# Kernel optimization log

Hardware: AMD Instinct MI355X
Metric: run time of the kernel (lower is better)

## Reference

```python
import jax, jax.numpy as jnp
import numpy as np

EPS = 1e-8
H = 4      # n_heads
W = 64     # mem_word_length


def _split_controls(controls):
    # per-head partition: [W, W, W, 1, 1, 3, 1]
    B = controls.shape[0]
    sizes = [W, W, W, 1, 1, 3, 1]
    parts, pos = [], 0
    for s in sizes:
        n = H * s
        parts.append(controls[:, pos:pos + n].reshape(B, H, s))
        pos += n
    return parts  # keys, erase_vec, write_vec, betas, gates, shifts, gammas


def _address_memory(memory, keys, betas, gates, shifts, gammas, prev_weights):
    keys = jnp.tanh(keys)                      # [B,H,W]
    betas = jax.nn.softplus(betas)             # [B,H,1]
    gates = jax.nn.sigmoid(gates)              # [B,H,1]
    shifts = jax.nn.softmax(shifts, axis=-1)   # [B,H,3]
    gammas = 1.0 + jax.nn.softplus(gammas)     # [B,H,1]

    # cosine similarity: [B,H,N]
    dots = jnp.einsum('bhw,bnw->bhn', keys, memory)
    norm = jnp.linalg.norm(keys, axis=-1, keepdims=True) \
         * jnp.linalg.norm(memory, axis=-1)[:, None, :]
    scores = dots / (norm + EPS)

    w_content = jax.nn.softmax(scores * betas, axis=-1)            # [B,H,N]
    w_interp = gates * w_content + (1.0 - gates) * prev_weights    # [B,H,N]

    # circular 3-tap shift: out[n] = s0*w[n-1] + s1*w[n] + s2*w[n+1]
    w_shift = (shifts[..., 0:1] * jnp.roll(w_interp, 1, axis=-1)
             + shifts[..., 1:2] * w_interp
             + shifts[..., 2:3] * jnp.roll(w_interp, -1, axis=-1))

    w_sharp = w_shift ** gammas
    return w_sharp / (jnp.sum(w_sharp, axis=-1, keepdims=True) + EPS)


def reference(memory, controls, prev_weights):
    keys, erase_vec, write_vec, betas, gates, shifts, gammas = _split_controls(controls)
    write_dist = _address_memory(memory, keys, betas, gates, shifts, gammas, prev_weights)  # [B,H,N]
    write_data = jnp.tanh(write_vec)       # [B,H,W]
    erase_data = jax.nn.sigmoid(erase_vec) # [B,H,W]

    # erase: prod over heads of (1 - w[b,h,n]*e[b,h,w]) -> [B,N,W]
    erase_matrix = jnp.prod(1.0 - write_dist[:, :, :, None] * erase_data[:, :, None, :], axis=1)
    update_matrix = jnp.einsum('bhn,bhw->bnw', write_dist, write_data)
    return memory * erase_matrix + update_matrix


def setup_inputs() -> dict:
    key = jax.random.key(0)
    k1, k2, k3 = jax.random.split(key, 3)
    B, N = 64, 8192
    memory = jax.random.normal(k1, (B, N, W), dtype=jnp.float32)
    controls = jax.random.normal(k2, (B, H * (3 * W + 6)), dtype=jnp.float32)
    prev_weights = jax.random.uniform(k3, (B, H, N), dtype=jnp.float32)
    return {"memory": memory, "controls": controls, "prev_weights": prev_weights}
```

## Files before the change

kernel.cpp:

```cpp
#include <hip/hip_runtime.h>
#include <math.h>

#define EPS 1e-8f

__device__ __forceinline__ float softplus_f(float x) {
    return (x > 20.0f) ? x : log1pf(expf(x));
}
__device__ __forceinline__ float sigmoid_f(float x) {
    return 1.0f / (1.0f + expf(-x));
}

__global__ void prep_kernel(const float* __restrict__ controls,
                            float* __restrict__ keys,
                            float* __restrict__ params,
                            float* __restrict__ erase,
                            float* __restrict__ writev)
{
    int b = blockIdx.x;
    int t = threadIdx.x;
    int h = t >> 6;
    int w = t & 63;
    const float* c = controls + (size_t)b * 792;

    float kt = tanhf(c[h * 64 + w]);
    int bh = b * 4 + h;
    keys[bh * 64 + w]   = kt;
    erase[bh * 64 + w]  = sigmoid_f(c[256 + h * 64 + w]);
    writev[bh * 64 + w] = tanhf(c[512 + h * 64 + w]);

    float nsq = kt * kt;
    #pragma unroll
    for (int m = 1; m < 64; m <<= 1) nsq += __shfl_xor(nsq, m, 64);

    if (w == 0) {
        float beta  = softplus_f(c[768 + h]);
        float gate  = sigmoid_f(c[772 + h]);
        float r0 = c[776 + h * 3 + 0];
        float r1 = c[776 + h * 3 + 1];
        float r2 = c[776 + h * 3 + 2];
        float mx = fmaxf(r0, fmaxf(r1, r2));
        float e0 = expf(r0 - mx), e1 = expf(r1 - mx), e2 = expf(r2 - mx);
        float inv = 1.0f / (e0 + e1 + e2);
        float gamma = 1.0f + softplus_f(c[788 + h]);
        float* p = params + bh * 8;
        p[0] = beta; p[1] = gate;
        p[2] = e0 * inv; p[3] = e1 * inv; p[4] = e2 * inv;
        p[5] = gamma; p[6] = sqrtf(nsq); p[7] = 0.0f;
    }
}

__global__ void score_kernel(const float* __restrict__ memory,
                             const float* __restrict__ keys,
                             const float* __restrict__ params,
                             float* __restrict__ scores, int N)
{
    int b = blockIdx.y;
    int nbase = blockIdx.x * 16;
    int t = threadIdx.x;
    int row = t >> 4;
    int lane = t & 15;
    int n = nbase + row;

    __shared__ float kk[4 * 64];
    __shared__ float betas[4], knorm[4];
    __shared__ float sc[4][16];

    kk[t] = keys[(size_t)b * 256 + t];
    if (t < 4) {
        betas[t] = params[((size_t)b * 4 + t) * 8 + 0];
        knorm[t] = params[((size_t)b * 4 + t) * 8 + 6];
    }
    __syncthreads();

    const float4 m4 = ((const float4*)(memory + ((size_t)b * N + n) * 64))[lane];
    float nsq = m4.x * m4.x + m4.y * m4.y + m4.z * m4.z + m4.w * m4.w;
    float d[4];
    #pragma unroll
    for (int h = 0; h < 4; h++) {
        float4 k4 = ((const float4*)(kk + h * 64))[lane];
        d[h] = m4.x * k4.x + m4.y * k4.y + m4.z * k4.z + m4.w * k4.w;
    }
    #pragma unroll
    for (int m = 1; m < 16; m <<= 1) {
        nsq += __shfl_xor(nsq, m, 64);
        #pragma unroll
        for (int h = 0; h < 4; h++) d[h] += __shfl_xor(d[h], m, 64);
    }
    if (lane == 0) {
        float mn = sqrtf(nsq);
        #pragma unroll
        for (int h = 0; h < 4; h++)
            sc[h][row] = betas[h] * d[h] / (mn * knorm[h] + EPS);
    }
    __syncthreads();
    if (t < 64) {
        int h = t >> 4, i = t & 15;
        scores[((size_t)b * 4 + h) * N + nbase + i] = sc[h][i];
    }
}

__device__ __forceinline__ float block_reduce_sum(float v, float* red) {
    #pragma unroll
    for (int m = 1; m < 64; m <<= 1) v += __shfl_xor(v, m, 64);
    int wid = threadIdx.x >> 6;
    __syncthreads();
    if ((threadIdx.x & 63) == 0) red[wid] = v;
    __syncthreads();
    float r = red[0];
    #pragma unroll
    for (int i = 1; i < 16; i++) r += red[i];
    return r;
}
__device__ __forceinline__ float block_reduce_max(float v, float* red) {
    #pragma unroll
    for (int m = 1; m < 64; m <<= 1) v = fmaxf(v, __shfl_xor(v, m, 64));
    int wid = threadIdx.x >> 6;
    __syncthreads();
    if ((threadIdx.x & 63) == 0) red[wid] = v;
    __syncthreads();
    float r = red[0];
    #pragma unroll
    for (int i = 1; i < 16; i++) r = fmaxf(r, red[i]);
    return r;
}

__global__ __launch_bounds__(1024)
void weights_kernel(float* __restrict__ scores,
                    const float* __restrict__ prev,
                    const float* __restrict__ params, int N)
{
    int bh = blockIdx.x;
    int t = threadIdx.x;
    const float* p = params + (size_t)bh * 8;
    float gate = p[1], s0 = p[2], s1 = p[3], s2 = p[4], gamma = p[5];

    __shared__ float wi_s[8192];
    __shared__ float red[16];

    float* srow = scores + (size_t)bh * N;
    const float* prow = prev + (size_t)bh * N;

    const int K = N / 1024;
    float sv[8];
    #pragma unroll
    for (int k = 0; k < 8; k++) sv[k] = srow[t + k * 1024];

    float mx = sv[0];
    #pragma unroll
    for (int k = 1; k < 8; k++) mx = fmaxf(mx, sv[k]);
    mx = block_reduce_max(mx, red);

    float e[8]; float lsum = 0.0f;
    #pragma unroll
    for (int k = 0; k < 8; k++) { e[k] = expf(sv[k] - mx); lsum += e[k]; }
    float S = block_reduce_sum(lsum, red);
    float invS = 1.0f / S;

    float om_gate = 1.0f - gate;
    #pragma unroll
    for (int k = 0; k < 8; k++) {
        int i = t + k * 1024;
        float wc = e[k] * invS;
        wi_s[i] = gate * wc + om_gate * prow[i];
    }
    __syncthreads();

    float wsv[8]; float lsum2 = 0.0f;
    #pragma unroll
    for (int k = 0; k < 8; k++) {
        int i = t + k * 1024;
        int im1 = (i == 0) ? (N - 1) : (i - 1);
        int ip1 = (i == N - 1) ? 0 : (i + 1);
        float wshift = s0 * wi_s[im1] + s1 * wi_s[i] + s2 * wi_s[ip1];
        float wp = powf(wshift, gamma);
        wsv[k] = wp; lsum2 += wp;
    }
    float T = block_reduce_sum(lsum2, red);
    float invT = 1.0f / (T + EPS);
    #pragma unroll
    for (int k = 0; k < 8; k++) srow[t + k * 1024] = wsv[k] * invT;
    (void)K;
}

__global__ void output_kernel(const float* __restrict__ memory,
                              const float* __restrict__ wdist,
                              const float* __restrict__ erase,
                              const float* __restrict__ writev,
                              float* __restrict__ out, int N)
{
    int t = threadIdx.x;
    int rowsPerB = N / 16;
    int b = blockIdx.x / rowsPerB;
    int nbase = (blockIdx.x % rowsPerB) * 16;

    __shared__ float es[256], wv[256];
    __shared__ float wd_s[4][16];
    es[t] = erase[(size_t)b * 256 + t];
    wv[t] = writev[(size_t)b * 256 + t];
    if (t < 64) {
        int h = t >> 4, i = t & 15;
        wd_s[h][i] = wdist[((size_t)b * 4 + h) * N + nbase + i];
    }
    __syncthreads();

    int row = t >> 4, lane = t & 15;
    int n = nbase + row;
    const float4 m4 = ((const float4*)(memory + ((size_t)b * N + n) * 64))[lane];

    float4 pe = make_float4(1.f, 1.f, 1.f, 1.f);
    float4 up = make_float4(0.f, 0.f, 0.f, 0.f);
    #pragma unroll
    for (int h = 0; h < 4; h++) {
        float f = wd_s[h][row];
        float4 e4 = ((const float4*)(es + h * 64))[lane];
        float4 w4 = ((const float4*)(wv + h * 64))[lane];
        pe.x *= 1.0f - f * e4.x;  pe.y *= 1.0f - f * e4.y;
        pe.z *= 1.0f - f * e4.z;  pe.w *= 1.0f - f * e4.w;
        up.x += f * w4.x;  up.y += f * w4.y;
        up.z += f * w4.z;  up.w += f * w4.w;
    }
    float4 o;
    o.x = m4.x * pe.x + up.x;
    o.y = m4.y * pe.y + up.y;
    o.z = m4.z * pe.z + up.z;
    o.w = m4.w * pe.w + up.w;
    ((float4*)(out + ((size_t)b * N + n) * 64))[lane] = o;
}

extern "C" void kernel_launch(void* const* d_in, const int* in_sizes, int n_in,
                              void* d_out, int out_size, void* d_ws, size_t ws_size,
                              hipStream_t stream) {
    const float* memory   = (const float*)d_in[0];
    const float* controls = (const float*)d_in[1];
    const float* prev     = (const float*)d_in[2];
    float* out = (float*)d_out;

    int B = in_sizes[1] / 792;
    int N = in_sizes[0] / (B * 64);

    float* wsf    = (float*)d_ws;
    float* keys   = wsf;
    float* params = keys   + (size_t)B * 256;
    float* erase  = params + (size_t)B * 32;
    float* writev = erase  + (size_t)B * 256;
    float* scores = writev + (size_t)B * 256;

    prep_kernel<<<B, 256, 0, stream>>>(controls, keys, params, erase, writev);
    score_kernel<<<dim3(N / 16, B), 256, 0, stream>>>(memory, keys, params, scores, N);
    weights_kernel<<<B * 4, 1024, 0, stream>>>(scores, prev, params, N);
    output_kernel<<<B * (N / 16), 256, 0, stream>>>(memory, scores, erase, writev, out, N);
}
```

Measured before the change: 283.0 us.

## Process 64 rows per block in score/output kernels, vectorize weights kernel

The score and output kernels now handle 64 memory rows per 256-thread block (four rows per thread) instead of 16. Each thread issues four float4 loads up front, and the keys, erase and write vectors are kept in registers and reused across those rows. This cuts block count and per-block setup such as the shared-memory staging and syncs, and gives more memory-level parallelism. The weights kernel switches to float4 loads and stores over two contiguous halves and replaces expf/powf with the fast __expf/__logf intrinsics, which trades some accuracy for fewer instructions.

Result: faster. 271.7 us (-4.0%).

```diff
diff --git a/kernel.cpp b/kernel.cpp
--- a/kernel.cpp
+++ b/kernel.cpp
@@ -49,21 +49,21 @@
     }
 }
 
-__global__ void score_kernel(const float* __restrict__ memory,
-                             const float* __restrict__ keys,
-                             const float* __restrict__ params,
-                             float* __restrict__ scores, int N)
+__global__ __launch_bounds__(256)
+void score_kernel(const float* __restrict__ memory,
+                  const float* __restrict__ keys,
+                  const float* __restrict__ params,
+                  float* __restrict__ scores, int N)
 {
     int b = blockIdx.y;
-    int nbase = blockIdx.x * 16;
-    int t = threadIdx.x;
-    int row = t >> 4;
+    int nbase = blockIdx.x * 64;
+    int t = threadIdx.x;
+    int rq = t >> 4;
     int lane = t & 15;
-    int n = nbase + row;
-
-    __shared__ float kk[4 * 64];
+
+    __shared__ float kk[256];
     __shared__ float betas[4], knorm[4];
-    __shared__ float sc[4][16];
+    __shared__ float sc[4][64];
 
     kk[t] = keys[(size_t)b * 256 + t];
     if (t < 4) {
@@ -72,31 +72,43 @@
     }
     __syncthreads();
 
-    const float4 m4 = ((const float4*)(memory + ((size_t)b * N + n) * 64))[lane];
-    float nsq = m4.x * m4.x + m4.y * m4.y + m4.z * m4.z + m4.w * m4.w;
-    float d[4];
-    #pragma unroll
-    for (int h = 0; h < 4; h++) {
-        float4 k4 = ((const float4*)(kk + h * 64))[lane];
-        d[h] = m4.x * k4.x + m4.y * k4.y + m4.z * k4.z + m4.w * k4.w;
-    }
-    #pragma unroll
-    for (int m = 1; m < 16; m <<= 1) {
-        nsq += __shfl_xor(nsq, m, 64);
-        #pragma unroll
-        for (int h = 0; h < 4; h++) d[h] += __shfl_xor(d[h], m, 64);
-    }
-    if (lane == 0) {
-        float mn = sqrtf(nsq);
-        #pragma unroll
-        for (int h = 0; h < 4; h++)
-            sc[h][row] = betas[h] * d[h] / (mn * knorm[h] + EPS);
-    }
-    __syncthreads();
-    if (t < 64) {
-        int h = t >> 4, i = t & 15;
-        scores[((size_t)b * 4 + h) * N + nbase + i] = sc[h][i];
-    }
+    float4 k4[4];
+    #pragma unroll
+    for (int h = 0; h < 4; h++) k4[h] = ((const float4*)(kk + h * 64))[lane];
+
+    float4 m4[4];
+    #pragma unroll
+    for (int j = 0; j < 4; j++) {
+        int n = nbase + rq + 16 * j;
+        m4[j] = ((const float4*)(memory + ((size_t)b * N + n) * 64))[lane];
+    }
+
+    #pragma unroll
+    for (int j = 0; j < 4; j++) {
+        float nsq = m4[j].x * m4[j].x + m4[j].y * m4[j].y
+                  + m4[j].z * m4[j].z + m4[j].w * m4[j].w;
+        float d[4];
+        #pragma unroll
+        for (int h = 0; h < 4; h++) {
+            d[h] = m4[j].x * k4[h].x + m4[j].y * k4[h].y
+                 + m4[j].z * k4[h].z + m4[j].w * k4[h].w;
+        }
+        #pragma unroll
+        for (int m = 1; m < 16; m <<= 1) {
+            nsq += __shfl_xor(nsq, m, 64);
+            #pragma unroll
+            for (int h = 0; h < 4; h++) d[h] += __shfl_xor(d[h], m, 64);
+        }
+        if (lane == 0) {
+            float mn = sqrtf(nsq);
+            int row = rq + 16 * j;
+            #pragma unroll
+            for (int h = 0; h < 4; h++)
+                sc[h][row] = betas[h] * d[h] / (mn * knorm[h] + EPS);
+        }
+    }
+    __syncthreads();
+    scores[((size_t)b * 4 + (t >> 6)) * N + nbase + (t & 63)] = sc[t >> 6][t & 63];
 }
 
 __device__ __forceinline__ float block_reduce_sum(float v, float* red) {
@@ -139,92 +151,112 @@
 
     float* srow = scores + (size_t)bh * N;
     const float* prow = prev + (size_t)bh * N;
-
-    const int K = N / 1024;
-    float sv[8];
-    #pragma unroll
-    for (int k = 0; k < 8; k++) sv[k] = srow[t + k * 1024];
-
-    float mx = sv[0];
-    #pragma unroll
-    for (int k = 1; k < 8; k++) mx = fmaxf(mx, sv[k]);
+    int half = N >> 1;
+    int i0 = 4 * t, i1 = half + 4 * t;
+
+    float4 sa = ((const float4*)srow)[t];
+    float4 sb = ((const float4*)srow)[half / 4 + t];
+    float4 pa = ((const float4*)prow)[t];
+    float4 pb = ((const float4*)prow)[half / 4 + t];
+
+    float mx = fmaxf(fmaxf(fmaxf(sa.x, sa.y), fmaxf(sa.z, sa.w)),
+                     fmaxf(fmaxf(sb.x, sb.y), fmaxf(sb.z, sb.w)));
     mx = block_reduce_max(mx, red);
 
-    float e[8]; float lsum = 0.0f;
-    #pragma unroll
-    for (int k = 0; k < 8; k++) { e[k] = expf(sv[k] - mx); lsum += e[k]; }
+    float ea[4] = { __expf(sa.x - mx), __expf(sa.y - mx), __expf(sa.z - mx), __expf(sa.w - mx) };
+    float eb[4] = { __expf(sb.x - mx), __expf(sb.y - mx), __expf(sb.z - mx), __expf(sb.w - mx) };
+    float lsum = ea[0] + ea[1] + ea[2] + ea[3] + eb[0] + eb[1] + eb[2] + eb[3];
     float S = block_reduce_sum(lsum, red);
     float invS = 1.0f / S;
 
-    float om_gate = 1.0f - gate;
-    #pragma unroll
-    for (int k = 0; k < 8; k++) {
-        int i = t + k * 1024;
-        float wc = e[k] * invS;
-        wi_s[i] = gate * wc + om_gate * prow[i];
+    float og = 1.0f - gate;
+    float pv_a[4] = { pa.x, pa.y, pa.z, pa.w };
+    float pv_b[4] = { pb.x, pb.y, pb.z, pb.w };
+    #pragma unroll
+    for (int k = 0; k < 4; k++) {
+        wi_s[i0 + k] = gate * (ea[k] * invS) + og * pv_a[k];
+        wi_s[i1 + k] = gate * (eb[k] * invS) + og * pv_b[k];
     }
     __syncthreads();
 
     float wsv[8]; float lsum2 = 0.0f;
     #pragma unroll
-    for (int k = 0; k < 8; k++) {
-        int i = t + k * 1024;
-        int im1 = (i == 0) ? (N - 1) : (i - 1);
-        int ip1 = (i == N - 1) ? 0 : (i + 1);
-        float wshift = s0 * wi_s[im1] + s1 * wi_s[i] + s2 * wi_s[ip1];
-        float wp = powf(wshift, gamma);
-        wsv[k] = wp; lsum2 += wp;
+    for (int c = 0; c < 2; c++) {
+        int base = (c == 0) ? i0 : i1;
+        #pragma unroll
+        for (int k = 0; k < 4; k++) {
+            int i = base + k;
+            int im1 = (i == 0) ? (N - 1) : (i - 1);
+            int ip1 = (i == N - 1) ? 0 : (i + 1);
+            float ws = s0 * wi_s[im1] + s1 * wi_s[i] + s2 * wi_s[ip1];
+            float wp = __expf(gamma * __logf(ws));
+            wsv[c * 4 + k] = wp; lsum2 += wp;
+        }
     }
     float T = block_reduce_sum(lsum2, red);
     float invT = 1.0f / (T + EPS);
-    #pragma unroll
-    for (int k = 0; k < 8; k++) srow[t + k * 1024] = wsv[k] * invT;
-    (void)K;
-}
-
-__global__ void output_kernel(const float* __restrict__ memory,
-                              const float* __restrict__ wdist,
-                              const float* __restrict__ erase,
-                              const float* __restrict__ writev,
-                              float* __restrict__ out, int N)
-{
-    int t = threadIdx.x;
-    int rowsPerB = N / 16;
-    int b = blockIdx.x / rowsPerB;
-    int nbase = (blockIdx.x % rowsPerB) * 16;
-
-    __shared__ float es[256], wv[256];
-    __shared__ float wd_s[4][16];
+
+    float4 oa = make_float4(wsv[0] * invT, wsv[1] * invT, wsv[2] * invT, wsv[3] * invT);
+    float4 ob = make_float4(wsv[4] * invT, wsv[5] * invT, wsv[6] * invT, wsv[7] * invT);
+    ((float4*)srow)[t] = oa;
+    ((float4*)srow)[half / 4 + t] = ob;
+}
+
+__global__ __launch_bounds__(256)
+void output_kernel(const float* __restrict__ memory,
+                   const float* __restrict__ wdist,
+                   const float* __restrict__ erase,
+                   const float* __restrict__ writev,
+                   float* __restrict__ out, int N)
+{
+    int t = threadIdx.x;
+    int blocksPerB = N >> 6;
+    int b = blockIdx.x / blocksPerB;
+    int nbase = (blockIdx.x % blocksPerB) << 6;
+
+    __shared__ float es[256], wv[256], wd_s[256];
     es[t] = erase[(size_t)b * 256 + t];
     wv[t] = writev[(size_t)b * 256 + t];
-    if (t < 64) {
-        int h = t >> 4, i = t & 15;
-        wd_s[h][i] = wdist[((size_t)b * 4 + h) * N + nbase + i];
-    }
-    __syncthreads();
-
-    int row = t >> 4, lane = t & 15;
-    int n = nbase + row;
-    const float4 m4 = ((const float4*)(memory + ((size_t)b * N + n) * 64))[lane];
-
-    float4 pe = make_float4(1.f, 1.f, 1.f, 1.f);
-    float4 up = make_float4(0.f, 0.f, 0.f, 0.f);
+    wd_s[t] = wdist[((size_t)b * 4 + (t >> 6)) * N + nbase + (t & 63)];
+    __syncthreads();
+
+    int rq = t >> 4, lane = t & 15;
+
+    float4 e4[4], w4[4];
     #pragma unroll
     for (int h = 0; h < 4; h++) {
-        float f = wd_s[h][row];
-        float4 e4 = ((const float4*)(es + h * 64))[lane];
-        float4 w4 = ((const float4*)(wv + h * 64))[lane];
-        pe.x *= 1.0f - f * e4.x;  pe.y *= 1.0f - f * e4.y;
-        pe.z *= 1.0f - f * e4.z;  pe.w *= 1.0f - f * e4.w;
-        up.x += f * w4.x;  up.y += f * w4.y;
-        up.z += f * w4.z;  up.w += f * w4.w;
-    }
-    float4 o;
-    o.x = m4.x * pe.x + up.x;
-    o.y = m4.y * pe.y + up.y;
-    o.z = m4.z * pe.z + up.z;
-    o.w = m4.w * pe.w + up.w;
-    ((float4*)(out + ((size_t)b * N + n) * 64))[lane] = o;
+        e4[h] = ((const float4*)(es + h * 64))[lane];
+        w4[h] = ((const float4*)(wv + h * 64))[lane];
+    }
+
+    float4 m4[4];
+    #pragma unroll
+    for (int j = 0; j < 4; j++) {
+        int n = nbase + rq + 16 * j;
+        m4[j] = ((const float4*)(memory + ((size_t)b * N + n) * 64))[lane];
+    }
+
+    #pragma unroll
+    for (int j = 0; j < 4; j++) {
+        int row = rq + 16 * j;
+        int n = nbase + row;
+        float4 pe = make_float4(1.f, 1.f, 1.f, 1.f);
+        float4 up = make_float4(0.f, 0.f, 0.f, 0.f);
+        #pragma unroll
+        for (int h = 0; h < 4; h++) {
+            float f = wd_s[h * 64 + row];
+            pe.x *= 1.0f - f * e4[h].x;  pe.y *= 1.0f - f * e4[h].y;
+            pe.z *= 1.0f - f * e4[h].z;  pe.w *= 1.0f - f * e4[h].w;
+            up.x += f * w4[h].x;  up.y += f * w4[h].y;
+            up.z += f * w4[h].z;  up.w += f * w4[h].w;
+        }
+        float4 o;
+        o.x = m4[j].x * pe.x + up.x;
+        o.y = m4[j].y * pe.y + up.y;
+        o.z = m4[j].z * pe.z + up.z;
+        o.w = m4[j].w * pe.w + up.w;
+        ((float4*)(out + ((size_t)b * N + n) * 64))[lane] = o;
+    }
 }
 
 extern "C" void kernel_launch(void* const* d_in, const int* in_sizes, int n_in,
@@ -246,7 +278,7 @@
     float* scores = writev + (size_t)B * 256;
 
     prep_kernel<<<B, 256, 0, stream>>>(controls, keys, params, erase, writev);
-    score_kernel<<<dim3(N / 16, B), 256, 0, stream>>>(memory, keys, params, scores, N);
+    score_kernel<<<dim3(N / 64, B), 256, 0, stream>>>(memory, keys, params, scores, N);
     weights_kernel<<<B * 4, 1024, 0, stream>>>(scores, prev, params, N);
-    output_kernel<<<B * (N / 16), 256, 0, stream>>>(memory, scores, erase, writev, out, N);
-}
+    output_kernel<<<B * (N / 64), 256, 0, stream>>>(memory, scores, erase, writev, out, N);
+}
```
